# Performance work log

Measured on AMD Instinct MI355X. Metric: run time of the kernel, lower is better.

The kernel has to match this reference:

```python
import jax, jax.numpy as jnp
import numpy as np

HIDDEN = 256
TOTAL_NUM = 32
VOCAB = TOTAL_NUM + 3  # BOS, EOS, PAD appended
IDX_PAD = TOTAL_NUM + 2
BETA = 1.0


def setup_inputs() -> dict:
    key = jax.random.key(0)
    k1, k2, k3, k4, k5 = jax.random.split(key, 5)
    B, P, T = 16, 8, 256
    event_obs = jax.random.randint(k1, (B, P, T), 0, VOCAB)
    dtime_obs = jax.random.uniform(k2, (B, P, T), dtype=jnp.float32)
    scale = 1.0 / np.sqrt(HIDDEN)
    Emb = jax.random.normal(k3, (VOCAB, HIDDEN), dtype=jnp.float32) * scale
    # CTLSTMCell: Linear(2H -> 7H) producing i, f, o, z, i_bar, f_bar, decay
    W = jax.random.normal(k4, (7 * HIDDEN, 2 * HIDDEN), dtype=jnp.float32) * scale
    b = jax.random.normal(k5, (7 * HIDDEN,), dtype=jnp.float32) * 0.01
    return {"event_obs": event_obs, "dtime_obs": dtime_obs, "Emb": Emb, "W": W, "b": b}


def _ct_lstm_right2left(event_obs, dtime_obs, Emb, W, b):
    B, P, T = event_obs.shape
    H = Emb.shape[1]
    dt = Emb.dtype
    emb_all = Emb[event_obs]  # [B,P,T,H]
    # steps process i = T-1 ... 1 (reverse); xs are time-major for i in [1, T-1]
    xs = (
        jnp.moveaxis(emb_all[:, :, 1:], 2, 0),      # [T-1,B,P,H]
        jnp.moveaxis(dtime_obs[:, :, 1:], 2, 0),    # [T-1,B,P]
        jnp.moveaxis(event_obs[:, :, 1:], 2, 0),    # [T-1,B,P]
    )
    init = (jnp.zeros((B, P, H), dt), jnp.zeros((B, P, H), dt), jnp.zeros((B, P, H), dt))

    def step(carry, x):
        c_plus, cbar_next, h_plus = carry
        emb_i, dtime_i, ev_i = x
        z = jnp.concatenate([emb_i, h_plus], axis=-1) @ W.T + b  # [B,P,7H]
        gi, gf, go, gz, gib, gfb, gd = jnp.split(z, 7, axis=-1)
        gi = jax.nn.sigmoid(gi)
        gf = jax.nn.sigmoid(gf)
        go = jax.nn.sigmoid(go)
        gz = jnp.tanh(gz)
        gib = jax.nn.sigmoid(gib)
        gfb = jax.nn.sigmoid(gfb)
        gd = jax.nn.softplus(BETA * gd) / BETA  # decay rate > 0
        cell_i = gf * c_plus + gi * gz
        cbar_i = gfb * cbar_next + gib * gz
        h_minus = go * jnp.tanh(cell_i)                       # decay(dt=0)
        decay = jnp.exp(-gd * dtime_i[..., None])
        c_im1 = cbar_i + (cell_i - cbar_i) * decay            # decay(dt=dtime_i)
        h_im1 = go * jnp.tanh(c_im1)
        mask = (ev_i != IDX_PAD).astype(dt)[..., None]
        c_im1 = c_im1 * mask
        cbar_i = cbar_i * mask
        h_im1 = h_im1 * mask
        ys = (cell_i, cbar_i, gd, go, h_im1, h_minus)
        return (c_im1, cbar_i, h_im1), ys

    _, ys = jax.lax.scan(step, init, xs, reverse=True)
    # ys[k] corresponds to i = k+1, matching torch's reversed append order
    return tuple(jnp.moveaxis(y, 0, 2) for y in ys)  # each [B,P,T-1,H]


def reference(event_obs, dtime_obs, Emb, W, b):
    all_cell, all_cell_bar, all_gate_decay, all_gate_output, all_hidden, all_hidden_after_update = \
        _ct_lstm_right2left(event_obs, dtime_obs, Emb, W, b)
    return (all_cell, all_cell_bar, all_gate_decay, all_gate_output, all_hidden, all_hidden_after_update)
```

## Files before the change

kernel.cpp:

```cpp
#include <hip/hip_runtime.h>
#include <cstddef>
#include <cstdint>


typedef _Float16 hf;
typedef _Float16 f16x8 __attribute__((ext_vector_type(8)));
typedef float    f32x4 __attribute__((ext_vector_type(4)));

#define HID  256
#define R7   1792
#define TT   256
#define NPAD 34
#define HBUF_HF 4096

__device__ __forceinline__ float sigf(float x) { return 1.0f / (1.0f + __expf(-x)); }
__device__ __forceinline__ float tanh_f(float x) { return 1.0f - 2.0f / (__expf(2.0f * x) + 1.0f); }
__device__ __forceinline__ float softplusf(float x) {
  return fmaxf(x, 0.0f) + __logf(1.0f + __expf(-fabsf(x)));
}

__global__ __launch_bounds__(256) void repack_mfma(const float* __restrict__ W,
                                                   f16x8* __restrict__ Wf) {
  int idx  = blockIdx.x * 256 + threadIdx.x;
  int lane = idx & 63;
  int kt   = (idx >> 6) & 7;
  int gb   = idx >> 9;
  int g    = gb % 7;
  int b    = gb / 7;
  int row  = g * HID + b * 16 + (lane & 15);
  int k0   = kt * 32 + (lane >> 4) * 8;
  const float* src = W + (size_t)row * 512 + 256 + k0;
  f16x8 o;
#pragma unroll
  for (int e = 0; e < 8; ++e) o[e] = (hf)src[e];
  Wf[idx] = o;
}

__global__ __launch_bounds__(256) void ew_kernel(const float* __restrict__ Emb,
                                                 const float* __restrict__ W,
                                                 const float* __restrict__ bias,
                                                 float* __restrict__ EW) {
  int wid  = (blockIdx.x * 256 + threadIdx.x) >> 6;
  int lane = threadIdx.x & 63;
  int o    = wid * 4;
#pragma unroll
  for (int qq = 0; qq < 4; ++qq, ++o) {
    int e = o / R7;
    int r = o - e * R7;
    const float4 ev4 = *(const float4*)(Emb + e * HID + lane * 4);
    const float4 wv4 = *(const float4*)(W + (size_t)r * 512 + lane * 4);
    float acc = ev4.x * wv4.x + ev4.y * wv4.y + ev4.z * wv4.z + ev4.w * wv4.w;
#pragma unroll
    for (int m = 32; m >= 1; m >>= 1) acc += __shfl_xor(acc, m, 64);
    if (lane == 0) EW[o] = acc + bias[r];
  }
}

__global__ __launch_bounds__(256, 1) void scan_mfma(
    const int* __restrict__ event, const float* __restrict__ dtime,
    const float* __restrict__ EW, const f16x8* __restrict__ Wf,
    hf* __restrict__ hbuf, int* __restrict__ flags,
    float* __restrict__ out) {
  const int tid = threadIdx.x;
  const int b   = blockIdx.x & 15;
  const int p   = blockIdx.x >> 4;
  const int j0  = b * 16;
  const int wid = tid >> 6, lane = tid & 63;
  const int seq = tid >> 4, jj = tid & 15;
  const int j   = j0 + jj;
  const int q   = lane >> 4, nn = lane & 15;

  __shared__ int   evs[32][TT];
  __shared__ float dts[32][TT];
  __shared__ __align__(16) float gbuf[7][16][20];
  __shared__ float ews[35 * 7 * 17];

#pragma unroll 4
  for (int r = 0; r < 32; ++r) {
    evs[r][tid] = event[(size_t)(p * 32 + r) * TT + tid];
    dts[r][tid] = dtime[(size_t)(p * 32 + r) * TT + tid];
  }
  for (int idx = tid; idx < 35 * 112; idx += 256) {
    int e  = idx / 112, r = idx - e * 112;
    int g  = r >> 4, n2 = r & 15;
    ews[(e * 7 + g) * 17 + n2] = EW[(size_t)e * R7 + g * HID + j0 + n2];
  }

  const int  g0  = 2 * wid;
  const bool two = (wid < 3);
  f16x8 B0[8], B1[8];
  {
    const f16x8* wsrc = Wf + (size_t)((b * 7 + g0) * 8) * 64 + lane;
#pragma unroll
    for (int kt = 0; kt < 8; ++kt) B0[kt] = wsrc[kt * 64];
    if (two) {
#pragma unroll
      for (int kt = 0; kt < 8; ++kt) B1[kt] = wsrc[(8 + kt) * 64];
    }
  }
  asm volatile("s_waitcnt vmcnt(0)" ::: "memory");
  __builtin_amdgcn_sched_barrier(0);
#pragma unroll
  for (int kt = 0; kt < 8; ++kt) {
    asm volatile("" :: "v"(B0[kt]));
    if (two) asm volatile("" :: "v"(B1[kt]));
  }
  __syncthreads();

  int* flb = flags + p * 64;
  hf*  hpb = hbuf + (size_t)p * 4 * HBUF_HF;

  const int off16 = ((j >> 5) * 64 + seq + 16 * ((j >> 3) & 3)) * 8 + (j & 7);
  const size_t OS = 8355840;

  float cp0 = 0.f, cb0 = 0.f, cp1 = 0.f, cb1 = 0.f;
  int pr = 0;

  auto body = [&](const int c, const int it, float& cp, float& cb) {
    const int   i   = 255 - it, t = i - 1;
    const int   cs  = c * 16 + seq;
    const int   ev  = evs[cs][i];
    const float dt  = dts[cs][i];
    const int   nc  = c ^ 1;
    const int   itn = (c == 0) ? it : it + 1;

    asm volatile("s_waitcnt vmcnt(6)" : "+v"(pr) :: "memory");
    __builtin_amdgcn_sched_barrier(0);
    __builtin_amdgcn_s_barrier();

    if (tid == 0 && itn > 0)
      __hip_atomic_store(&flb[nc * 32 + b], itn, __ATOMIC_RELAXED,
                         __HIP_MEMORY_SCOPE_AGENT);

    if (it > 0) {
      int pv = (nn == b) ? 0x7fffffff : pr;
      if (!__all(pv >= it)) {
        int gd = 0;
        for (;;) {
          int v = (nn == b) ? 0x7fffffff
                : __hip_atomic_load(&flb[c * 32 + nn], __ATOMIC_RELAXED,
                                    __HIP_MEMORY_SCOPE_AGENT);
          if (__all(v >= it) || ++gd > (1 << 20)) break;
        }
      }
    }

    f16x8 av[8];
    if (it > 0) {
      const hf* hp = hpb + (size_t)(c * 2 + (it & 1)) * HBUF_HF + (size_t)lane * 8;
#pragma unroll
      for (int kt = 0; kt < 8; ++kt)
        asm volatile("global_load_dwordx4 %0, %1, off sc0 sc1"
                     : "=v"(av[kt]) : "v"(hp + (size_t)kt * 512) : "memory");
    }

    float e0[4], e1[4];
#pragma unroll
    for (int r = 0; r < 4; ++r) {
      const int evr  = evs[c * 16 + 4 * q + r][i];
      const int base = (evr * 7 + g0) * 17 + nn;
      e0[r] = ews[base];
      e1[r] = two ? ews[base + 17] : 0.0f;
    }

    asm volatile("s_waitcnt vmcnt(0)" ::: "memory");
    __builtin_amdgcn_sched_barrier(0);
    if (it > 0) {
#pragma unroll
      for (int kt = 0; kt < 8; ++kt) asm volatile("" : "+v"(av[kt]));
    }

    f32x4 acc0 = {e0[0], e0[1], e0[2], e0[3]};
    f32x4 acc1 = {e1[0], e1[1], e1[2], e1[3]};
    if (it > 0) {
#pragma unroll
      for (int kt = 0; kt < 8; ++kt) {
        acc0 = __builtin_amdgcn_mfma_f32_16x16x32_f16(av[kt], B0[kt], acc0, 0, 0, 0);
        if (two)
          acc1 = __builtin_amdgcn_mfma_f32_16x16x32_f16(av[kt], B1[kt], acc1, 0, 0, 0);
      }
    }

    *(f32x4*)&gbuf[g0][nn][4 * q] = acc0;
    if (two) *(f32x4*)&gbuf[g0 + 1][nn][4 * q] = acc1;
    asm volatile("s_waitcnt lgkmcnt(0)" ::: "memory");
    __builtin_amdgcn_s_barrier();
    __builtin_amdgcn_sched_barrier(0);

    float zz[7];
#pragma unroll
    for (int g = 0; g < 7; ++g) zz[g] = gbuf[g][jj][seq];
    float gi = sigf(zz[0]), gf = sigf(zz[1]), go = sigf(zz[2]);
    float gz = tanh_f(zz[3]);
    float gib = sigf(zz[4]), gfb = sigf(zz[5]);
    float gd = softplusf(zz[6]);
    float cell = gf * cp + gi * gz;
    float cbar = gfb * cb + gib * gz;
    float hm   = go * tanh_f(cell);
    float dec  = __expf(-gd * dt);
    float cim  = cbar + (cell - cbar) * dec;
    float him  = go * tanh_f(cim);
    float msk  = (ev != NPAD) ? 1.0f : 0.0f;
    float cbm  = cbar * msk;
    float hn   = him * msk;
    cp = cim * msk;
    cb = cbm;

    unsigned short hb16 = __builtin_bit_cast(unsigned short, (hf)hn);
    unsigned nb = __shfl_down((unsigned)hb16, 1, 64);
    if (it < 254 && !(jj & 1)) {
      unsigned pack = (unsigned)hb16 | (nb << 16);
      hf* hw = hpb + (size_t)(c * 2 + ((it + 1) & 1)) * HBUF_HF;
      asm volatile("global_store_dword %0, %1, off sc0 sc1"
                   :: "v"((unsigned*)(hw + off16)), "v"(pack) : "memory");
    }

    asm volatile("global_load_dword %0, %1, off sc0 sc1"
                 : "=v"(pr) : "v"(flb + nc * 32 + nn) : "memory");

    float* o = out + (size_t)(p * 32 + cs) * 65280 + (size_t)t * HID + j;
    asm volatile("global_store_dword %0, %1, off" :: "v"(o), "v"(cell) : "memory");
    asm volatile("global_store_dword %0, %1, off" :: "v"(o + OS), "v"(cbm) : "memory");
    asm volatile("global_store_dword %0, %1, off" :: "v"(o + 2 * OS), "v"(gd) : "memory");
    asm volatile("global_store_dword %0, %1, off" :: "v"(o + 3 * OS), "v"(go) : "memory");
    asm volatile("global_store_dword %0, %1, off" :: "v"(o + 4 * OS), "v"(hn) : "memory");
    asm volatile("global_store_dword %0, %1, off" :: "v"(o + 5 * OS), "v"(hm) : "memory");
  };

#pragma unroll 1
  for (int it = 0; it < 255; ++it) {
    body(0, it, cp0, cb0);
    body(1, it, cp1, cb1);
  }
}

extern "C" void kernel_launch(void* const* d_in, const int* in_sizes, int n_in,
                              void* d_out, int out_size, void* d_ws, size_t ws_size,
                              hipStream_t stream) {
  const int*   event = (const int*)d_in[0];
  const float* dtime = (const float*)d_in[1];
  const float* Emb   = (const float*)d_in[2];
  const float* W     = (const float*)d_in[3];
  const float* bias  = (const float*)d_in[4];
  float*       out   = (float*)d_out;

  char*  ws = (char*)d_ws;
  f16x8* Wf = (f16x8*)ws;
  float* EW = (float*)(ws + 917504);
  hf*    hb = (hf*)(ws + 917504 + 250880);
  int*   fl = (int*)(ws + 917504 + 250880 + 131072);

  hipMemsetAsync(ws + 917504 + 250880, 0, 131072 + 1024, stream);
  repack_mfma<<<224, 256, 0, stream>>>(W, Wf);
  ew_kernel<<<3920, 256, 0, stream>>>(Emb, W, bias, EW);
  scan_mfma<<<64, 256, 0, stream>>>(event, dtime, EW, Wf, hb, fl, out);
}
```

Before: 1.002 ms.

## Interleave four sequence chunks per block and prefetch hidden state one quarter ahead

The scan kernel now gives each block 64 sequences in four chunks of 16 instead of two chunks of 32, and halves the grid to 32 blocks. The next chunk's hidden-state load is issued right after the current chunk's store, so cross-block communication latency overlaps with other chunks' work. Events are stored as bytes in shared memory to fit the larger tiles. The EW precompute is also restructured to stage Emb in LDS and loop over vocab per W row. The risk is fewer active CUs and a more intricate flag/buffer protocol that may hide ordering bugs.

```diff
diff --git a/kernel.cpp b/kernel.cpp
--- a/kernel.cpp
+++ b/kernel.cpp
@@ -11,7 +11,6 @@
 #define R7   1792
 #define TT   256
 #define NPAD 34
-#define HBUF_HF 4096
 
 __device__ __forceinline__ float sigf(float x) { return 1.0f / (1.0f + __expf(-x)); }
 __device__ __forceinline__ float tanh_f(float x) { return 1.0f - 2.0f / (__expf(2.0f * x) + 1.0f); }
@@ -40,19 +39,23 @@
                                                  const float* __restrict__ W,
                                                  const float* __restrict__ bias,
                                                  float* __restrict__ EW) {
-  int wid  = (blockIdx.x * 256 + threadIdx.x) >> 6;
-  int lane = threadIdx.x & 63;
-  int o    = wid * 4;
-#pragma unroll
-  for (int qq = 0; qq < 4; ++qq, ++o) {
-    int e = o / R7;
-    int r = o - e * R7;
-    const float4 ev4 = *(const float4*)(Emb + e * HID + lane * 4);
+  __shared__ float embl[35 * 256];
+  const int tid = threadIdx.x;
+  for (int idx = tid; idx < 35 * 256; idx += 256) embl[idx] = Emb[idx];
+  __syncthreads();
+  const int wid = tid >> 6, lane = tid & 63;
+  int r = blockIdx.x * 16 + wid * 4;
+#pragma unroll
+  for (int rr = 0; rr < 4; ++rr, ++r) {
     const float4 wv4 = *(const float4*)(W + (size_t)r * 512 + lane * 4);
-    float acc = ev4.x * wv4.x + ev4.y * wv4.y + ev4.z * wv4.z + ev4.w * wv4.w;
-#pragma unroll
-    for (int m = 32; m >= 1; m >>= 1) acc += __shfl_xor(acc, m, 64);
-    if (lane == 0) EW[o] = acc + bias[r];
+    const float brr = bias[r];
+    for (int e = 0; e < 35; ++e) {
+      const float4 em = *(const float4*)(embl + e * 256 + lane * 4);
+      float acc = wv4.x * em.x + wv4.y * em.y + wv4.z * em.z + wv4.w * em.w;
+#pragma unroll
+      for (int m = 32; m >= 1; m >>= 1) acc += __shfl_xor(acc, m, 64);
+      if (lane == 0) EW[(size_t)e * R7 + r] = acc + brr;
+    }
   }
 }
 
@@ -70,15 +73,15 @@
   const int j   = j0 + jj;
   const int q   = lane >> 4, nn = lane & 15;
 
-  __shared__ int   evs[32][TT];
-  __shared__ float dts[32][TT];
+  __shared__ uint8_t evs8[64][TT];
+  __shared__ float   dts[64][TT];
   __shared__ __align__(16) float gbuf[7][16][20];
-  __shared__ float ews[35 * 7 * 17];
+  __shared__ float   ews[35 * 7 * 17];
 
 #pragma unroll 4
-  for (int r = 0; r < 32; ++r) {
-    evs[r][tid] = event[(size_t)(p * 32 + r) * TT + tid];
-    dts[r][tid] = dtime[(size_t)(p * 32 + r) * TT + tid];
+  for (int r = 0; r < 64; ++r) {
+    evs8[r][tid] = (uint8_t)event[(size_t)(p * 64 + r) * TT + tid];
+    dts[r][tid]  = dtime[(size_t)(p * 64 + r) * TT + tid];
   }
   for (int idx = tid; idx < 35 * 112; idx += 256) {
     int e  = idx / 112, r = idx - e * 112;
@@ -107,72 +110,67 @@
   }
   __syncthreads();
 
-  int* flb = flags + p * 64;
-  hf*  hpb = hbuf + (size_t)p * 4 * HBUF_HF;
+  int* flp = flags + p * 64;
+  hf*  hpb = hbuf + (size_t)p * 8 * 4096;
 
   const int off16 = ((j >> 5) * 64 + seq + 16 * ((j >> 3) & 3)) * 8 + (j & 7);
   const size_t OS = 8355840;
 
   float cp0 = 0.f, cb0 = 0.f, cp1 = 0.f, cb1 = 0.f;
+  float cp2 = 0.f, cb2 = 0.f, cp3 = 0.f, cb3 = 0.f;
+  f16x8 avE[8], avO[8];
+#pragma unroll
+  for (int kt = 0; kt < 8; ++kt) { avE[kt] = (f16x8)(hf)0.0f; avO[kt] = (f16x8)(hf)0.0f; }
   int pr = 0;
 
-  auto body = [&](const int c, const int it, float& cp, float& cb) {
-    const int   i   = 255 - it, t = i - 1;
-    const int   cs  = c * 16 + seq;
-    const int   ev  = evs[cs][i];
-    const float dt  = dts[cs][i];
-    const int   nc  = c ^ 1;
-    const int   itn = (c == 0) ? it : it + 1;
-
-    asm volatile("s_waitcnt vmcnt(6)" : "+v"(pr) :: "memory");
+  auto quarter = [&](const int c, const int it, f16x8 (&av)[8],
+                     float& cp, float& cb) {
+    const int i   = 255 - it;
+    const int cs  = c * 16 + seq;
+    const int c2  = (c + 2) & 3;
+    const int it2 = it + (c >= 2 ? 1 : 0);
+    const int c3  = (c + 3) & 3;
+    const int v1  = (c == 0) ? it : it + 1;
+
+    asm volatile("s_waitcnt vmcnt(14)" : "+v"(pr) :: "memory");
     __builtin_amdgcn_sched_barrier(0);
     __builtin_amdgcn_s_barrier();
-
-    if (tid == 0 && itn > 0)
-      __hip_atomic_store(&flb[nc * 32 + b], itn, __ATOMIC_RELAXED,
-                         __HIP_MEMORY_SCOPE_AGENT);
-
-    if (it > 0) {
+    __builtin_amdgcn_sched_barrier(0);
+
+    if (tid == 0 && v1 > 0)
+      asm volatile("global_store_dword %0, %1, off sc0 sc1"
+                   :: "v"(flp + c3 * 16 + b), "v"(v1) : "memory");
+
+    if (it2 >= 1 && it2 <= 254) {
       int pv = (nn == b) ? 0x7fffffff : pr;
-      if (!__all(pv >= it)) {
+      if (!__all(pv >= it2)) {
         int gd = 0;
+        const int* fp = flp + c2 * 16 + nn;
         for (;;) {
-          int v = (nn == b) ? 0x7fffffff
-                : __hip_atomic_load(&flb[c * 32 + nn], __ATOMIC_RELAXED,
-                                    __HIP_MEMORY_SCOPE_AGENT);
-          if (__all(v >= it) || ++gd > (1 << 20)) break;
+          int v;
+          asm volatile("global_load_dword %0, %1, off sc0 sc1\n\t"
+                       "s_waitcnt vmcnt(0)" : "=v"(v) : "v"(fp) : "memory");
+          v = (nn == b) ? 0x7fffffff : v;
+          if (__all(v >= it2) || ++gd > (1 << 20)) break;
         }
       }
     }
 
-    f16x8 av[8];
-    if (it > 0) {
-      const hf* hp = hpb + (size_t)(c * 2 + (it & 1)) * HBUF_HF + (size_t)lane * 8;
-#pragma unroll
-      for (int kt = 0; kt < 8; ++kt)
-        asm volatile("global_load_dwordx4 %0, %1, off sc0 sc1"
-                     : "=v"(av[kt]) : "v"(hp + (size_t)kt * 512) : "memory");
-    }
+    asm volatile("global_load_dword %0, %1, off sc0 sc1"
+                 : "=v"(pr) : "v"(flp + c3 * 16 + nn) : "memory");
 
     float e0[4], e1[4];
 #pragma unroll
     for (int r = 0; r < 4; ++r) {
-      const int evr  = evs[c * 16 + 4 * q + r][i];
+      const int evr  = evs8[c * 16 + 4 * q + r][i];
       const int base = (evr * 7 + g0) * 17 + nn;
       e0[r] = ews[base];
       e1[r] = two ? ews[base + 17] : 0.0f;
     }
-
-    asm volatile("s_waitcnt vmcnt(0)" ::: "memory");
-    __builtin_amdgcn_sched_barrier(0);
-    if (it > 0) {
-#pragma unroll
-      for (int kt = 0; kt < 8; ++kt) asm volatile("" : "+v"(av[kt]));
-    }
-
     f32x4 acc0 = {e0[0], e0[1], e0[2], e0[3]};
     f32x4 acc1 = {e1[0], e1[1], e1[2], e1[3]};
-    if (it > 0) {
+
+    if (it >= 1) {
 #pragma unroll
       for (int kt = 0; kt < 8; ++kt) {
         acc0 = __builtin_amdgcn_mfma_f32_16x16x32_f16(av[kt], B0[kt], acc0, 0, 0, 0);
@@ -187,6 +185,8 @@
     __builtin_amdgcn_s_barrier();
     __builtin_amdgcn_sched_barrier(0);
 
+    const int   ev = evs8[cs][i];
+    const float dt = dts[cs][i];
     float zz[7];
 #pragma unroll
     for (int g = 0; g < 7; ++g) zz[g] = gbuf[g][jj][seq];
@@ -206,19 +206,27 @@
     cp = cim * msk;
     cb = cbm;
 
-    unsigned short hb16 = __builtin_bit_cast(unsigned short, (hf)hn);
-    unsigned nb = __shfl_down((unsigned)hb16, 1, 64);
-    if (it < 254 && !(jj & 1)) {
-      unsigned pack = (unsigned)hb16 | (nb << 16);
-      hf* hw = hpb + (size_t)(c * 2 + ((it + 1) & 1)) * HBUF_HF;
-      asm volatile("global_store_dword %0, %1, off sc0 sc1"
-                   :: "v"((unsigned*)(hw + off16)), "v"(pack) : "memory");
-    }
-
-    asm volatile("global_load_dword %0, %1, off sc0 sc1"
-                 : "=v"(pr) : "v"(flb + nc * 32 + nn) : "memory");
-
-    float* o = out + (size_t)(p * 32 + cs) * 65280 + (size_t)t * HID + j;
+    {
+      unsigned short hb16 = __builtin_bit_cast(unsigned short, (hf)hn);
+      unsigned nb = __shfl_down((unsigned)hb16, 1, 64);
+      if (!(jj & 1)) {
+        unsigned pack = (unsigned)hb16 | (nb << 16);
+        hf* hw = hpb + (size_t)(c * 2 + ((it + 1) & 1)) * 4096;
+        asm volatile("global_store_dword %0, %1, off sc0 sc1"
+                     :: "v"((unsigned*)(hw + off16)), "v"(pack) : "memory");
+      }
+    }
+
+    {
+      const int itc = (it2 > 254) ? 254 : it2;
+      const hf* hp = hpb + (size_t)(c2 * 2 + (itc & 1)) * 4096 + (size_t)lane * 8;
+#pragma unroll
+      for (int kt = 0; kt < 8; ++kt)
+        asm volatile("global_load_dwordx4 %0, %1, off sc0 sc1"
+                     : "=v"(av[kt]) : "v"(hp + (size_t)kt * 512) : "memory");
+    }
+
+    float* o = out + (size_t)(p * 64 + cs) * 65280 + (size_t)(i - 1) * HID + j;
     asm volatile("global_store_dword %0, %1, off" :: "v"(o), "v"(cell) : "memory");
     asm volatile("global_store_dword %0, %1, off" :: "v"(o + OS), "v"(cbm) : "memory");
     asm volatile("global_store_dword %0, %1, off" :: "v"(o + 2 * OS), "v"(gd) : "memory");
@@ -229,8 +237,10 @@
 
 #pragma unroll 1
   for (int it = 0; it < 255; ++it) {
-    body(0, it, cp0, cb0);
-    body(1, it, cp1, cb1);
+    quarter(0, it, avE, cp0, cb0);
+    quarter(1, it, avO, cp1, cb1);
+    quarter(2, it, avE, cp2, cb2);
+    quarter(3, it, avO, cp3, cb3);
   }
 }
 
@@ -250,8 +260,8 @@
   hf*    hb = (hf*)(ws + 917504 + 250880);
   int*   fl = (int*)(ws + 917504 + 250880 + 131072);
 
-  hipMemsetAsync(ws + 917504 + 250880, 0, 131072 + 1024, stream);
+  hipMemsetAsync(ws + 917504 + 250880, 0, 131072 + 512, stream);
   repack_mfma<<<224, 256, 0, stream>>>(W, Wf);
-  ew_kernel<<<3920, 256, 0, stream>>>(Emb, W, bias, EW);
-  scan_mfma<<<64, 256, 0, stream>>>(event, dtime, EW, Wf, hb, fl, out);
-}
+  ew_kernel<<<112, 256, 0, stream>>>(Emb, W, bias, EW);
+  scan_mfma<<<32, 256, 0, stream>>>(event, dtime, EW, Wf, hb, fl, out);
+}
```

After: 2.003 ms. 99.9% more time.
